# Optimization experiments

Hardware: AMD Instinct MI355X
Metric: run time of the kernel (lower is better)

Reference implementation:

```python
import jax, jax.numpy as jnp
import numpy as np

B, CIN, H, W = 16, 16, 320, 320
OUT, KS, K = 16, 3, 4
HIDDEN = int(CIN * 0.25) + 1  # 5, matches attention2d
PAD = 1


def setup_inputs() -> dict:
    key = jax.random.key(0)
    k1, k2, k3, k4 = jax.random.split(key, 4)
    x = jax.random.normal(k1, (B, CIN, H, W), dtype=jnp.float32)
    # attention2d params: fc1 (1x1 conv, no bias), fc2 (1x1 conv, bias)
    w1 = jax.random.normal(k2, (HIDDEN, CIN), dtype=jnp.float32) * (2.0 / CIN) ** 0.5
    w2 = jax.random.normal(k3, (K * OUT, HIDDEN), dtype=jnp.float32) * (2.0 / HIDDEN) ** 0.5
    b2 = jnp.zeros((K * OUT,), dtype=jnp.float32)
    # expert weight bank [out, in//groups, ks, ks, K]
    weight = jax.random.normal(k4, (OUT, CIN, KS, KS, K), dtype=jnp.float32) * (1.0 / (CIN * KS * KS)) ** 0.5
    return {"x": x, "w1": w1, "w2": w2, "b2": b2, "weight": weight}


def reference(x, w1, w2, b2, weight):
    b, cin, h, w = x.shape
    out_p, cin_g, ks, _, kk = weight.shape
    # attention2d: global avg pool -> 1x1 conv -> relu -> 1x1 conv (+bias)
    pooled = x.mean(axis=(2, 3))                       # [B, Cin]
    hid = jax.nn.relu(pooled @ w1.T)                   # [B, hidden]
    attn = hid @ w2.T + b2                             # [B, K*out]
    # softmax over K experts per output channel
    s = jax.nn.softmax(attn.reshape(b, kk, out_p), axis=1)  # [B, K, out]
    # faithful to the torch conv2d grouping trick: flat layout is (k, o),
    # then group o consumes flat channels [o*K:(o+1)*K]
    coeffs = s.reshape(b, -1).reshape(b, out_p, kk)    # [B, out, K]
    # per-sample mixed kernels
    wmix = jnp.einsum('bok,ocxyk->bocxy', coeffs, weight)  # [B, out, in//g, ks, ks]
    # per-sample grouped conv via feature_group_count = B * groups (groups=1)
    xg = x.reshape(1, b * cin, h, w)
    wg = wmix.reshape(b * out_p, cin_g, ks, ks)
    out = jax.lax.conv_general_dilated(
        xg, wg, window_strides=(1, 1), padding=((PAD, PAD), (PAD, PAD)),
        feature_group_count=b, dimension_numbers=('NCHW', 'OIHW', 'NCHW'))
    return out.reshape(b, out_p, out.shape[-2], out.shape[-1])
```

## Files before the change

kernel.cpp:

```cpp
#include <hip/hip_runtime.h>
#include <hip/hip_bf16.h>
#include <math.h>

#define BB   16
#define CIN  16
#define HH   320
#define WW   320
#define OUTC 16
#define KK   4
#define HID  5
#define HWSZ (HH * WW)

#define TW   64
#define TH   16
#define LROW 68
#define LROWS 18
#define LDSN (LROWS * LROW * CIN)
#define KCH  5

typedef __attribute__((ext_vector_type(8))) short bf16x8_t;
typedef __attribute__((ext_vector_type(4))) float f32x4_t;

static __device__ __forceinline__ unsigned short f2bf(float f) {
    union { float f; unsigned u; } x; x.f = f;
    unsigned r = x.u + 0x7FFF + ((x.u >> 16) & 1);
    return (unsigned short)(r >> 16);
}

__global__ __launch_bounds__(1024)
void dg_pool_kernel(const float* __restrict__ x, float* __restrict__ pooled) {
    const int plane = blockIdx.x;
    const float4* p4 = (const float4*)(x + (size_t)plane * HWSZ);
    float s = 0.f;
    #pragma unroll 5
    for (int i = threadIdx.x; i < HWSZ / 4; i += 1024) {
        float4 v = p4[i];
        s += (v.x + v.y) + (v.z + v.w);
    }
    #pragma unroll
    for (int off = 32; off > 0; off >>= 1) s += __shfl_down(s, off, 64);
    __shared__ float red[16];
    if ((threadIdx.x & 63) == 0) red[threadIdx.x >> 6] = s;
    __syncthreads();
    if (threadIdx.x == 0) {
        float t = 0.f;
        #pragma unroll
        for (int i = 0; i < 16; ++i) t += red[i];
        pooled[plane] = t * (1.f / (float)HWSZ);
    }
}

__global__ __launch_bounds__(64)
void dg_mix_kernel(const float* __restrict__ pooled,
                   const float* __restrict__ w1,
                   const float* __restrict__ w2,
                   const float* __restrict__ b2,
                   const float* __restrict__ weight,
                   unsigned short* __restrict__ wB) {
    const int b = blockIdx.x;
    const int tid = threadIdx.x;
    __shared__ float sm[64];
    __shared__ float coeff[64];

    float pb[CIN];
    #pragma unroll
    for (int c = 0; c < CIN; ++c) pb[c] = pooled[b * CIN + c];
    float hid[HID];
    #pragma unroll
    for (int h = 0; h < HID; ++h) {
        float a = 0.f;
        #pragma unroll
        for (int c = 0; c < CIN; ++c) a = fmaf(pb[c], w1[h * CIN + c], a);
        hid[h] = fmaxf(a, 0.f);
    }
    float a = b2[tid];
    #pragma unroll
    for (int h = 0; h < HID; ++h) a = fmaf(hid[h], w2[tid * HID + h], a);
    sm[tid] = a;
    __syncthreads();

    const int oa = tid & 15;
    float a0 = sm[oa], a1 = sm[16 + oa], a2 = sm[32 + oa], a3 = sm[48 + oa];
    float m = fmaxf(fmaxf(a0, a1), fmaxf(a2, a3));
    float denom = expf(a0 - m) + expf(a1 - m) + expf(a2 - m) + expf(a3 - m);
    coeff[tid] = expf(sm[tid] - m) / denom;
    __syncthreads();

    const int o = tid & 15;
    const int kbase = (tid >> 4) * 8;
    #pragma unroll
    for (int kc = 0; kc < KCH; ++kc) {
        unsigned short frag[8];
        #pragma unroll
        for (int j = 0; j < 8; ++j) {
            const int k = kc * 32 + kbase + j;
            float v = 0.f;
            if (k < 144) {
                const int tap = k >> 4;
                const int c = k & 15;
                const float* wp = weight + (((size_t)(o * CIN + c) * 9 + tap) << 2);
                v = coeff[o * 4 + 0] * wp[0] + coeff[o * 4 + 1] * wp[1]
                  + coeff[o * 4 + 2] * wp[2] + coeff[o * 4 + 3] * wp[3];
            }
            frag[j] = f2bf(v);
        }
        unsigned short* dst = wB + (((size_t)(b * KCH + kc) * 64) + tid) * 8;
        #pragma unroll
        for (int j = 0; j < 8; ++j) dst[j] = frag[j];
    }
}

__global__ __launch_bounds__(256, 2)
void dg_conv_kernel(const float* __restrict__ x,
                    const unsigned short* __restrict__ wB,
                    float* __restrict__ out) {
    const int b   = blockIdx.z;
    const int by0 = blockIdx.y * TH;
    const int bx0 = blockIdx.x * TW;
    const int tid = threadIdx.x;
    const int lane = tid & 63;
    const int wave = tid >> 6;

    __shared__ __align__(16) unsigned short sx[LDSN];

    bf16x8_t Bf[KCH];
    {
        const unsigned short* wBb = wB + (size_t)b * KCH * 512;
        #pragma unroll
        for (int kc = 0; kc < KCH; ++kc)
            Bf[kc] = *(const bf16x8_t*)(wBb + kc * 512 + lane * 8);
    }

    {
        const float* xb = x + (size_t)b * CIN * HWSZ;
        #pragma unroll 1
        for (int it = 0; it < 10; ++it) {
            const int t = tid + it * 256;
            if (t < 8 * LROWS * 17) {
                const int qx  = t % 17;
                const int t2  = t / 17;
                const int row = t2 % LROWS;
                const int cp  = t2 / LROWS;
                const int gy  = by0 - 1 + row;
                const bool vy = ((unsigned)gy < HH);
                const float* xr0 = xb + (size_t)(2 * cp) * HWSZ + (size_t)gy * WW;
                #pragma unroll
                for (int j = 0; j < 4; ++j) {
                    const int xx = qx * 4 + j;
                    const int gx = bx0 - 1 + xx;
                    const bool v = vy && ((unsigned)gx < WW);
                    const float v0 = v ? xr0[gx] : 0.f;
                    const float v1 = v ? xr0[HWSZ + gx] : 0.f;
                    const unsigned packed =
                        (unsigned)f2bf(v0) | ((unsigned)f2bf(v1) << 16);
                    const int P = row * LROW + xx;
                    const int idx = P * 16 + (((cp >> 2) ^ (P & 1)) << 3) + (cp & 3) * 2;
                    *(unsigned*)&sx[idx] = packed;
                }
            }
        }
    }

    const int m     = lane & 15;
    const int quad  = lane >> 4;
    const int chalf = quad & 1;
    int dP[KCH];
    #pragma unroll
    for (int kc = 0; kc < KCH; ++kc) {
        int t = 2 * kc + (quad >> 1);
        if (t > 8) t = 8;
        dP[kc] = (t / 3 - 1) * LROW + (t % 3 - 1);
    }

    f32x4_t acc[16];
    #pragma unroll
    for (int i = 0; i < 16; ++i) acc[i] = (f32x4_t){0.f, 0.f, 0.f, 0.f};

    __syncthreads();

    #pragma unroll
    for (int rr = 0; rr < 4; ++rr) {
        #pragma unroll
        for (int tx = 0; tx < 4; ++tx) {
            const int P0 = (4 * wave + rr + 1) * LROW + 1 + tx * 16 + m;
            #pragma unroll
            for (int kc = 0; kc < KCH; ++kc) {
                const int P = P0 + dP[kc];
                const int idx = P * 16 + ((chalf ^ (P & 1)) << 3);
                const bf16x8_t Af = *(const bf16x8_t*)&sx[idx];
                acc[rr * 4 + tx] = __builtin_amdgcn_mfma_f32_16x16x32_bf16(
                    Af, Bf[kc], acc[rr * 4 + tx], 0, 0, 0);
            }
        }
    }

    const int n = lane & 15;
    float* ob = out + ((size_t)(b * OUTC + n)) * HWSZ;
    #pragma unroll
    for (int rr = 0; rr < 4; ++rr) {
        const int gy = by0 + 4 * wave + rr;
        #pragma unroll
        for (int tx = 0; tx < 4; ++tx) {
            const int gx = bx0 + tx * 16 + quad * 4;
            *(f32x4_t*)(ob + (size_t)gy * WW + gx) = acc[rr * 4 + tx];
        }
    }
}

extern "C" void kernel_launch(void* const* d_in, const int* in_sizes, int n_in,
                              void* d_out, int out_size, void* d_ws, size_t ws_size,
                              hipStream_t stream) {
    const float* x      = (const float*)d_in[0];
    const float* w1     = (const float*)d_in[1];
    const float* w2     = (const float*)d_in[2];
    const float* b2     = (const float*)d_in[3];
    const float* weight = (const float*)d_in[4];
    float* out = (float*)d_out;

    float* pooled = (float*)d_ws;
    unsigned short* wBf = (unsigned short*)((float*)d_ws + 256);

    dg_pool_kernel<<<BB * CIN, 1024, 0, stream>>>(x, pooled);
    dg_mix_kernel<<<BB, 64, 0, stream>>>(pooled, w1, w2, b2, weight, wBf);
    dg_conv_kernel<<<dim3(WW / TW, HH / TH, BB), 256, 0, stream>>>(x, wBf, out);
}
```

Measured before the change: 250.8 us.

## Split LDS input tile into channel-half planes with 16-byte per-pixel loads

Restructures the shared-memory input tile from an interleaved 16-channel-per-pixel layout with XOR swizzle into two separate planes of 8 channels each. Each thread now gathers 8 channels for one pixel and writes a single 16-byte vector, and the MFMA A-fragment reads become plain contiguous 16-byte loads. The row pitch shrinks from 68 to 66, reducing LDS footprint, and launch bounds ask for 4 blocks per CU instead of 2. Global loads are now strided across channel planes per thread, which may coalesce worse, and dropping the swizzle may introduce LDS bank conflicts.

```diff
diff --git a/kernel.cpp b/kernel.cpp
--- a/kernel.cpp
+++ b/kernel.cpp
@@ -13,9 +13,11 @@
 
 #define TW   64
 #define TH   16
-#define LROW 68
+#define LROW 66
 #define LROWS 18
-#define LDSN (LROWS * LROW * CIN)
+#define NPIX (LROWS * LROW)
+#define NTASK (2 * NPIX)
+#define LDSN (2 * NPIX * 8)
 #define KCH  5
 
 typedef __attribute__((ext_vector_type(8))) short bf16x8_t;
@@ -110,7 +112,7 @@
     }
 }
 
-__global__ __launch_bounds__(256, 2)
+__global__ __launch_bounds__(256, 4)
 void dg_conv_kernel(const float* __restrict__ x,
                     const unsigned short* __restrict__ wB,
                     float* __restrict__ out) {
@@ -136,27 +138,25 @@
         #pragma unroll 1
         for (int it = 0; it < 10; ++it) {
             const int t = tid + it * 256;
-            if (t < 8 * LROWS * 17) {
-                const int qx  = t % 17;
-                const int t2  = t / 17;
-                const int row = t2 % LROWS;
-                const int cp  = t2 / LROWS;
-                const int gy  = by0 - 1 + row;
-                const bool vy = ((unsigned)gy < HH);
-                const float* xr0 = xb + (size_t)(2 * cp) * HWSZ + (size_t)gy * WW;
+            if (t < NTASK) {
+                const int half = (t >= NPIX) ? 1 : 0;
+                const int P    = t - half * NPIX;
+                const int row  = P / LROW;
+                const int px   = P - row * LROW;
+                const int gy = by0 - 1 + row;
+                const int gx = bx0 - 1 + px;
+                const bool valid = ((unsigned)gy < HH) && ((unsigned)gx < WW);
+                const int gyc = valid ? gy : 0;
+                const int gxc = valid ? gx : 0;
+                const float* bp = xb + (size_t)(half * 8) * HWSZ
+                                     + (size_t)gyc * WW + gxc;
+                bf16x8_t v8;
                 #pragma unroll
-                for (int j = 0; j < 4; ++j) {
-                    const int xx = qx * 4 + j;
-                    const int gx = bx0 - 1 + xx;
-                    const bool v = vy && ((unsigned)gx < WW);
-                    const float v0 = v ? xr0[gx] : 0.f;
-                    const float v1 = v ? xr0[HWSZ + gx] : 0.f;
-                    const unsigned packed =
-                        (unsigned)f2bf(v0) | ((unsigned)f2bf(v1) << 16);
-                    const int P = row * LROW + xx;
-                    const int idx = P * 16 + (((cp >> 2) ^ (P & 1)) << 3) + (cp & 3) * 2;
-                    *(unsigned*)&sx[idx] = packed;
+                for (int j = 0; j < 8; ++j) {
+                    float v = valid ? bp[(size_t)j * HWSZ] : 0.f;
+                    v8[j] = (short)f2bf(v);
                 }
+                *(bf16x8_t*)&sx[(size_t)t * 8] = v8;
             }
         }
     }
@@ -171,6 +171,7 @@
         if (t > 8) t = 8;
         dP[kc] = (t / 3 - 1) * LROW + (t % 3 - 1);
     }
+    const int hofs = chalf * NPIX;
 
     f32x4_t acc[16];
     #pragma unroll
@@ -185,9 +186,8 @@
             const int P0 = (4 * wave + rr + 1) * LROW + 1 + tx * 16 + m;
             #pragma unroll
             for (int kc = 0; kc < KCH; ++kc) {
-                const int P = P0 + dP[kc];
-                const int idx = P * 16 + ((chalf ^ (P & 1)) << 3);
-                const bf16x8_t Af = *(const bf16x8_t*)&sx[idx];
+                const int S = hofs + P0 + dP[kc];
+                const bf16x8_t Af = *(const bf16x8_t*)&sx[(size_t)S * 8];
                 acc[rr * 4 + tx] = __builtin_amdgcn_mfma_f32_16x16x32_bf16(
                     Af, Bf[kc], acc[rr * 4 + tx], 0, 0, 0);
             }
```

Result: faster. 242.5 us (-3.3%).
